# Performance work log

Measured on AMD Instinct MI355X. Metric: run time of the kernel, lower is better.

Reference implementation:

```python
import jax, jax.numpy as jnp
import numpy as np

EMBEDDING_DIM = 64
N_EMBEDDINGS = 512


def setup_inputs() -> dict:
    key = jax.random.key(0)
    k1, k2 = jax.random.split(key)
    inputs = jax.random.normal(k1, (32, 64, 64, 64), dtype=jnp.float32)  # NCHW, C==embedding_dim
    weight = jax.random.normal(k2, (N_EMBEDDINGS, EMBEDDING_DIM), dtype=jnp.float32)
    return {"inputs": inputs, "weight": weight}


def reference(inputs, weight):
    # NCHW -> NHWC, flatten to [N, D]
    x = jnp.transpose(inputs, (0, 2, 3, 1))  # [B, H, W, D]
    in_shape = x.shape
    flat = x.reshape(-1, EMBEDDING_DIM)  # [N, D]

    distances = (
        jnp.sum(flat * flat, axis=1, keepdims=True)
        + jnp.sum(weight * weight, axis=1)
        - 2.0 * flat @ weight.T
    )
    idx = jnp.argmin(distances, axis=1)  # [N]

    # one-hot @ weight is just a gather
    quantized = weight[idx].reshape(in_shape)  # [B, H, W, D]

    # commitment loss: mse(stop_grad(quantized), x)
    e_latent_loss = jnp.mean(jnp.square(jax.lax.stop_gradient(quantized) - x))

    # straight-through estimator
    quantized = x + jax.lax.stop_gradient(quantized - x)

    return jnp.transpose(quantized, (0, 3, 1, 2)), e_latent_loss
```

## Files before the change

### kernel.cpp

```cpp
#include <hip/hip_runtime.h>
#include <math.h>

typedef short bf16x8 __attribute__((ext_vector_type(8)));
typedef float f32x4 __attribute__((ext_vector_type(4)));

#define VQ_D 64
#define VQ_K 512
#define VQ_NQ 131072
#define VQ_TOTAL 8388608
#define NCK 8
#define TAU 8e-3f

typedef __attribute__((address_space(1))) void as1_void;
typedef __attribute__((address_space(3))) void as3_void;

__device__ __forceinline__ void gll16(const void* g, void* l) {
    __builtin_amdgcn_global_load_lds((as1_void*)(void*)g, (as3_void*)l, 16, 0, 0);
}
__device__ __forceinline__ void gll4(const void* g, void* l) {
    __builtin_amdgcn_global_load_lds((as1_void*)(void*)g, (as3_void*)l, 4, 0, 0);
}

__device__ __forceinline__ ushort bf16_rne(float f) {
    uint u = __builtin_bit_cast(uint, f);
    u += 0x7fffu + ((u >> 16) & 1u);
    return (ushort)(u >> 16);
}
__device__ __forceinline__ float bf16_to_f(ushort h) {
    uint u = ((uint)h) << 16;
    return __builtin_bit_cast(float, u);
}
__device__ __forceinline__ uint rne_top(float r) {
    uint t = __builtin_bit_cast(uint, r);
    return t + 0x7fffu + ((t >> 16) & 1u);
}
__device__ __forceinline__ uint pack_hi16(uint a, uint b) {
    return __builtin_amdgcn_perm(b, a, 0x07060302u);
}

__global__ __launch_bounds__(128) void vq_prep(const float* __restrict__ w,
                                               ushort* __restrict__ wfrag,
                                               float* __restrict__ wn,
                                               float* __restrict__ out) {
    if (blockIdx.x == 0 && threadIdx.x == 0) out[VQ_TOTAL] = 0.f;
    const int tid = threadIdx.x;
    const int k = (blockIdx.x << 4) + (tid >> 3);
    const int g = tid & 7;
    const float4* row = (const float4*)(w + k * VQ_D);
    float4 a = row[2 * g], b4 = row[2 * g + 1];
    float v[8] = {a.x, a.y, a.z, a.w, b4.x, b4.y, b4.z, b4.w};
    ushort hi[8], lo[8];
    float nrm = 0.f;
#pragma unroll
    for (int j = 0; j < 8; ++j) {
        nrm = fmaf(v[j], v[j], nrm);
        hi[j] = bf16_rne(v[j]);
        lo[j] = bf16_rne(v[j] - bf16_to_f(hi[j]));
    }
    nrm += __shfl_xor(nrm, 1, 64);
    nrm += __shfl_xor(nrm, 2, 64);
    nrm += __shfl_xor(nrm, 4, 64);
    if (g == 0) wn[k] = nrm;
    const int t = k >> 4, col = k & 15;
    const int quad = g & 3, fh = g >> 2;
    bf16x8* basez = (bf16x8*)wfrag + t * 256 + quad * 16 + col;
    basez[fh * 64]       = *(bf16x8*)hi;
    basez[(2 + fh) * 64] = *(bf16x8*)lo;
}

__global__ __launch_bounds__(512, 4) void vq_main(const float* __restrict__ in,
                                                  const float* __restrict__ w,
                                                  const ushort* __restrict__ wfrag,
                                                  const float* __restrict__ wng,
                                                  float* __restrict__ out) {
    __shared__ __align__(16) char bstage[2][16384];
    __shared__ float wn_lds[VQ_K];
    __shared__ float xn_lds[128];
    __shared__ float pb_lds[2][128], ps_lds[2][128];
    __shared__ int   pi_lds[2][128], pj_lds[2][128];
    __shared__ int   bi_lds[128];
    __shared__ double loss_lds[8];

    const int tid  = threadIdx.x;
    const int lane = tid & 63;
    const int wid  = tid >> 6;
    const int qg   = wid >> 1;
    const int cg   = wid & 1;
    const int col  = lane & 15;
    const int quad = lane >> 4;
    const int n0  = blockIdx.x * 128;
    const int b   = n0 >> 12;
    const int hw0 = n0 & 4095;
    const float* xg0 = in + (b << 18) + hw0;

    {
        const char* gs = (const char*)wfrag + tid * 16;
        char* lb = &bstage[0][0] + wid * 1024;
        gll16(gs, lb);
        gll16(gs + 8192, lb + 8192);
        gll4(wng + tid, (char*)wn_lds + wid * 256);
    }

    bf16x8 ah0[2], ah1[2], al0[2], al1[2];
#pragma unroll
    for (int T = 0; T < 2; ++T) {
        const float* xq = xg0 + qg * 32 + T * 16 + col;
        float sx = 0.f;
        uint AH0[4], AL0[4], AH1[4], AL1[4];
#pragma unroll
        for (int m = 0; m < 4; ++m) {
            float a0 = xq[(quad * 8 + 2 * m) << 12];
            float b0 = xq[(quad * 8 + 2 * m + 1) << 12];
            float a1 = xq[(32 + quad * 8 + 2 * m) << 12];
            float b1 = xq[(32 + quad * 8 + 2 * m + 1) << 12];
            sx = fmaf(a0, a0, sx); sx = fmaf(b0, b0, sx);
            sx = fmaf(a1, a1, sx); sx = fmaf(b1, b1, sx);
            uint ua0 = __builtin_bit_cast(uint, a0), ub0 = __builtin_bit_cast(uint, b0);
            uint ua1 = __builtin_bit_cast(uint, a1), ub1 = __builtin_bit_cast(uint, b1);
            AH0[m] = pack_hi16(ua0, ub0);
            AH1[m] = pack_hi16(ua1, ub1);
            float ha0 = __builtin_bit_cast(float, ua0 & 0xFFFF0000u);
            float hb0 = __builtin_bit_cast(float, ub0 & 0xFFFF0000u);
            float ha1 = __builtin_bit_cast(float, ua1 & 0xFFFF0000u);
            float hb1 = __builtin_bit_cast(float, ub1 & 0xFFFF0000u);
            AL0[m] = pack_hi16(rne_top(a0 - ha0), rne_top(b0 - hb0));
            AL1[m] = pack_hi16(rne_top(a1 - ha1), rne_top(b1 - hb1));
        }
        ah0[T] = *(bf16x8*)AH0; al0[T] = *(bf16x8*)AL0;
        ah1[T] = *(bf16x8*)AH1; al1[T] = *(bf16x8*)AL1;
        sx += __shfl_xor(sx, 16, 64);
        sx += __shfl_xor(sx, 32, 64);
        if (quad == 0) xn_lds[qg * 32 + T * 16 + col] = sx;
    }

    __syncthreads();

    float best[2][4], sec[2][4];
#pragma unroll
    for (int T = 0; T < 2; ++T)
#pragma unroll
        for (int r = 0; r < 4; ++r) { best[T][r] = 3.0e38f; sec[T][r] = 3.0e38f; }

#pragma unroll 1
    for (int c = 0; c < NCK; ++c) {
        char* const bcur = &bstage[c & 1][0];
        if (c + 1 < NCK) {
            const char* gs = (const char*)wfrag + (c + 1) * 16384 + tid * 16;
            char* lb = &bstage[(c + 1) & 1][0] + wid * 1024;
            gll16(gs, lb);
            gll16(gs + 8192, lb + 8192);
        }
#pragma unroll
        for (int s = 0; s < 2; ++s) {
            const int st = cg * 2 + s;
            const int t2 = 4 * c + st;
            const char* rb = bcur + st * 4096 + lane * 16;
            bf16x8 bh0 = *(const bf16x8*)(rb);
            bf16x8 bh1 = *(const bf16x8*)(rb + 1024);
            bf16x8 bl0 = *(const bf16x8*)(rb + 2048);
            bf16x8 bl1 = *(const bf16x8*)(rb + 3072);
            const float wnv = wn_lds[t2 * 16 + col];
#pragma unroll
            for (int T = 0; T < 2; ++T) {
                f32x4 acc = {0.f, 0.f, 0.f, 0.f};
                __builtin_amdgcn_s_setprio(1);
                acc = __builtin_amdgcn_mfma_f32_16x16x32_bf16(ah0[T], bh0, acc, 0, 0, 0);
                acc = __builtin_amdgcn_mfma_f32_16x16x32_bf16(ah1[T], bh1, acc, 0, 0, 0);
                acc = __builtin_amdgcn_mfma_f32_16x16x32_bf16(ah0[T], bl0, acc, 0, 0, 0);
                acc = __builtin_amdgcn_mfma_f32_16x16x32_bf16(ah1[T], bl1, acc, 0, 0, 0);
                acc = __builtin_amdgcn_mfma_f32_16x16x32_bf16(al0[T], bh0, acc, 0, 0, 0);
                acc = __builtin_amdgcn_mfma_f32_16x16x32_bf16(al1[T], bh1, acc, 0, 0, 0);
                __builtin_amdgcn_s_setprio(0);
#pragma unroll
                for (int j = 0; j < 4; ++j) {
                    float dist = fmaf(-2.f, acc[j], wnv);
                    uint u = (__builtin_bit_cast(uint, dist) & 0xFFFFFFE0u)
                           | ((uint)t2 & 0x1Fu);
                    float key = __builtin_bit_cast(float, u);
                    float m = fmaxf(best[T][j], key);
                    best[T][j] = fminf(best[T][j], key);
                    sec[T][j]  = fminf(sec[T][j], m);
                }
            }
        }
        __syncthreads();
    }

    float bD[2][4], sD[2][4];
    int bI[2][4], sI[2][4];
#pragma unroll
    for (int T = 0; T < 2; ++T)
#pragma unroll
    for (int r = 0; r < 4; ++r) {
        uint ub = __builtin_bit_cast(uint, best[T][r]);
        uint us = __builtin_bit_cast(uint, sec[T][r]);
        bI[T][r] = (int)(ub & 31u) * 16 + col;
        sI[T][r] = (int)(us & 31u) * 16 + col;
        bD[T][r] = __builtin_bit_cast(float, ub & 0xFFFFFFE0u);
        sD[T][r] = __builtin_bit_cast(float, us & 0xFFFFFFE0u);
    }

#pragma unroll
    for (int off = 1; off < 16; off <<= 1) {
#pragma unroll
        for (int T = 0; T < 2; ++T)
#pragma unroll
        for (int r = 0; r < 4; ++r) {
            float ob = __shfl_xor(bD[T][r], off, 64);
            float os = __shfl_xor(sD[T][r], off, 64);
            int   oi = __shfl_xor(bI[T][r], off, 64);
            int   oc = __shfl_xor(sI[T][r], off, 64);
            bool oWins = (ob < bD[T][r]) || (ob == bD[T][r] && oi < bI[T][r]);
            float nb  = oWins ? ob       : bD[T][r];
            int   ni  = oWins ? oi       : bI[T][r];
            float c1  = oWins ? bD[T][r] : ob;
            int   ci1 = oWins ? bI[T][r] : oi;
            float c2  = oWins ? os       : sD[T][r];
            int   ci2 = oWins ? oc       : sI[T][r];
            bool c1w = (c1 < c2) || (c1 == c2 && ci1 < ci2);
            sD[T][r] = c1w ? c1  : c2;
            sI[T][r] = c1w ? ci1 : ci2;
            bD[T][r] = nb; bI[T][r] = ni;
        }
    }
    if (col == 0) {
#pragma unroll
        for (int T = 0; T < 2; ++T)
#pragma unroll
        for (int r = 0; r < 4; ++r) {
            const int q = qg * 32 + T * 16 + quad * 4 + r;
            pb_lds[cg][q] = bD[T][r]; ps_lds[cg][q] = sD[T][r];
            pi_lds[cg][q] = bI[T][r]; pj_lds[cg][q] = sI[T][r];
        }
    }
    __syncthreads();

    {
        const int q = tid >> 2, part = tid & 3;
        float b0 = pb_lds[0][q], b1 = pb_lds[1][q];
        float s0 = ps_lds[0][q], s1 = ps_lds[1][q];
        int   i0 = pi_lds[0][q], i1 = pi_lds[1][q];
        int   j0 = pj_lds[0][q], j1 = pj_lds[1][q];
        bool w0 = (b0 < b1) || (b0 == b1 && i0 < i1);
        float cb  = w0 ? b0 : b1;  int cbi = w0 ? i0 : i1;
        float c1  = w0 ? b1 : b0;  int ci1 = w0 ? i1 : i0;
        float c2  = w0 ? s0 : s1;  int ci2 = w0 ? j0 : j1;
        bool c1w = (c1 < c2) || (c1 == c2 && ci1 < ci2);
        float cs  = c1w ? c1 : c2; int csi = c1w ? ci1 : ci2;

        double chosen = (double)cb;
        if (cs - cb < TAU) {
            const float* wb  = w + cbi * VQ_D + part * 16;
            const float* ws2 = w + csi * VQ_D + part * 16;
            const float* xqp = xg0 + q;
            double nb = 0.0, dotb = 0.0, ns = 0.0, dots = 0.0;
#pragma unroll
            for (int d0 = 0; d0 < 16; ++d0) {
                const int d = part * 16 + d0;
                double xv = (double)xqp[d << 12];
                double wbv = (double)wb[d0], wsv = (double)ws2[d0];
                nb = fma(wbv, wbv, nb); dotb = fma(xv, wbv, dotb);
                ns = fma(wsv, wsv, ns); dots = fma(xv, wsv, dots);
            }
#pragma unroll
            for (int off = 1; off < 4; off <<= 1) {
                nb   += __shfl_xor(nb,   off, 64);
                dotb += __shfl_xor(dotb, off, 64);
                ns   += __shfl_xor(ns,   off, 64);
                dots += __shfl_xor(dots, off, 64);
            }
            double db = nb - 2.0 * dotb, ds = ns - 2.0 * dots;
            if (ds < db || (ds == db && csi < cbi)) { cbi = csi; chosen = ds; }
            else                                    { chosen = db; }
        }
        if (part == 0) bi_lds[q] = cbi;
        double lq = (part == 0) ? ((double)xn_lds[q] + chosen) : 0.0;
#pragma unroll
        for (int off = 32; off > 0; off >>= 1)
            lq += __shfl_down(lq, off, 64);
        if (lane == 0) loss_lds[wid] = lq;
    }
    __syncthreads();
    if (tid == 0) {
        double s = 0.0;
#pragma unroll
        for (int wv = 0; wv < 8; ++wv) s += loss_lds[wv];
        atomicAdd(out + VQ_TOTAL, (float)(s * (1.0 / (double)VQ_TOTAL)));
    }

    {
        const int q = tid & 127, quarter = tid >> 7;
        const float4* wrow = (const float4*)(w + bi_lds[q] * VQ_D) + quarter * 4;
        float* op = out + (b << 18) + hw0 + q;
#pragma unroll
        for (int u = 0; u < 4; ++u) {
            float4 v = wrow[u];
            const int d = quarter * 16 + 4 * u;
            op[(d + 0) << 12] = v.x;
            op[(d + 1) << 12] = v.y;
            op[(d + 2) << 12] = v.z;
            op[(d + 3) << 12] = v.w;
        }
    }
}

extern "C" void kernel_launch(void* const* d_in, const int* in_sizes, int n_in,
                              void* d_out, int out_size, void* d_ws, size_t ws_size,
                              hipStream_t stream) {
    const float* in = (const float*)d_in[0];
    const float* w  = (const float*)d_in[1];
    float* out = (float*)d_out;

    ushort* wfrag = (ushort*)d_ws;
    float*  wn    = (float*)((char*)d_ws + 131072);

    vq_prep<<<32, 128, 0, stream>>>(w, wfrag, wn, out);
    vq_main<<<VQ_NQ / 128, 512, 0, stream>>>(in, w, wfrag, wn, out);
}
```

Before: 126.4 us.

## Give each wave the full codebook and double queries per block

Each block now processes 256 queries instead of 128, and every wave scans all 512 codebook entries for its own 32 queries instead of splitting the codebook between two waves. This halves the codebook staging and LDS fragment reads per query and removes the cross-wave best/second-best merge through LDS. The second-best update is also folded into a single fmed3 instruction. In exchange the grid shrinks to half as many blocks, which lowers the number of resident waves available to hide latency, and each wave runs a longer serial MFMA loop.

```diff
diff --git a/kernel.cpp b/kernel.cpp
--- a/kernel.cpp
+++ b/kernel.cpp
@@ -9,6 +9,7 @@
 #define VQ_NQ 131072
 #define VQ_TOTAL 8388608
 #define NCK 8
+#define QB 256
 #define TAU 8e-3f
 
 typedef __attribute__((address_space(1))) void as1_void;
@@ -75,20 +76,17 @@
                                                   float* __restrict__ out) {
     __shared__ __align__(16) char bstage[2][16384];
     __shared__ float wn_lds[VQ_K];
-    __shared__ float xn_lds[128];
-    __shared__ float pb_lds[2][128], ps_lds[2][128];
-    __shared__ int   pi_lds[2][128], pj_lds[2][128];
-    __shared__ int   bi_lds[128];
+    __shared__ float xn_lds[QB];
+    __shared__ float best_lds[QB], sec_lds[QB];
+    __shared__ int   bi_lds[QB], si_lds[QB];
     __shared__ double loss_lds[8];
 
     const int tid  = threadIdx.x;
     const int lane = tid & 63;
     const int wid  = tid >> 6;
-    const int qg   = wid >> 1;
-    const int cg   = wid & 1;
     const int col  = lane & 15;
     const int quad = lane >> 4;
-    const int n0  = blockIdx.x * 128;
+    const int n0  = blockIdx.x * QB;
     const int b   = n0 >> 12;
     const int hw0 = n0 & 4095;
     const float* xg0 = in + (b << 18) + hw0;
@@ -104,7 +102,7 @@
     bf16x8 ah0[2], ah1[2], al0[2], al1[2];
 #pragma unroll
     for (int T = 0; T < 2; ++T) {
-        const float* xq = xg0 + qg * 32 + T * 16 + col;
+        const float* xq = xg0 + wid * 32 + T * 16 + col;
         float sx = 0.f;
         uint AH0[4], AL0[4], AH1[4], AL1[4];
 #pragma unroll
@@ -130,7 +128,7 @@
         ah1[T] = *(bf16x8*)AH1; al1[T] = *(bf16x8*)AL1;
         sx += __shfl_xor(sx, 16, 64);
         sx += __shfl_xor(sx, 32, 64);
-        if (quad == 0) xn_lds[qg * 32 + T * 16 + col] = sx;
+        if (quad == 0) xn_lds[wid * 32 + T * 16 + col] = sx;
     }
 
     __syncthreads();
@@ -151,10 +149,9 @@
             gll16(gs + 8192, lb + 8192);
         }
 #pragma unroll
-        for (int s = 0; s < 2; ++s) {
-            const int st = cg * 2 + s;
-            const int t2 = 4 * c + st;
-            const char* rb = bcur + st * 4096 + lane * 16;
+        for (int s = 0; s < 4; ++s) {
+            const int t2 = 4 * c + s;
+            const char* rb = bcur + s * 4096 + lane * 16;
             bf16x8 bh0 = *(const bf16x8*)(rb);
             bf16x8 bh1 = *(const bf16x8*)(rb + 1024);
             bf16x8 bl0 = *(const bf16x8*)(rb + 2048);
@@ -177,9 +174,8 @@
                     uint u = (__builtin_bit_cast(uint, dist) & 0xFFFFFFE0u)
                            | ((uint)t2 & 0x1Fu);
                     float key = __builtin_bit_cast(float, u);
-                    float m = fmaxf(best[T][j], key);
+                    sec[T][j]  = __builtin_amdgcn_fmed3f(best[T][j], sec[T][j], key);
                     best[T][j] = fminf(best[T][j], key);
-                    sec[T][j]  = fminf(sec[T][j], m);
                 }
             }
         }
@@ -228,47 +224,35 @@
         for (int T = 0; T < 2; ++T)
 #pragma unroll
         for (int r = 0; r < 4; ++r) {
-            const int q = qg * 32 + T * 16 + quad * 4 + r;
-            pb_lds[cg][q] = bD[T][r]; ps_lds[cg][q] = sD[T][r];
-            pi_lds[cg][q] = bI[T][r]; pj_lds[cg][q] = sI[T][r];
+            const int q = wid * 32 + T * 16 + quad * 4 + r;
+            best_lds[q] = bD[T][r]; sec_lds[q] = sD[T][r];
+            bi_lds[q] = bI[T][r];   si_lds[q] = sI[T][r];
         }
     }
     __syncthreads();
 
     {
-        const int q = tid >> 2, part = tid & 3;
-        float b0 = pb_lds[0][q], b1 = pb_lds[1][q];
-        float s0 = ps_lds[0][q], s1 = ps_lds[1][q];
-        int   i0 = pi_lds[0][q], i1 = pi_lds[1][q];
-        int   j0 = pj_lds[0][q], j1 = pj_lds[1][q];
-        bool w0 = (b0 < b1) || (b0 == b1 && i0 < i1);
-        float cb  = w0 ? b0 : b1;  int cbi = w0 ? i0 : i1;
-        float c1  = w0 ? b1 : b0;  int ci1 = w0 ? i1 : i0;
-        float c2  = w0 ? s0 : s1;  int ci2 = w0 ? j0 : j1;
-        bool c1w = (c1 < c2) || (c1 == c2 && ci1 < ci2);
-        float cs  = c1w ? c1 : c2; int csi = c1w ? ci1 : ci2;
-
+        const int q = tid >> 1, part = tid & 1;
+        float cb = best_lds[q], cs = sec_lds[q];
+        int cbi = bi_lds[q], csi = si_lds[q];
         double chosen = (double)cb;
         if (cs - cb < TAU) {
-            const float* wb  = w + cbi * VQ_D + part * 16;
-            const float* ws2 = w + csi * VQ_D + part * 16;
+            const float* wb  = w + cbi * VQ_D + part * 32;
+            const float* ws2 = w + csi * VQ_D + part * 32;
             const float* xqp = xg0 + q;
             double nb = 0.0, dotb = 0.0, ns = 0.0, dots = 0.0;
 #pragma unroll
-            for (int d0 = 0; d0 < 16; ++d0) {
-                const int d = part * 16 + d0;
+            for (int d0 = 0; d0 < 32; ++d0) {
+                const int d = part * 32 + d0;
                 double xv = (double)xqp[d << 12];
                 double wbv = (double)wb[d0], wsv = (double)ws2[d0];
                 nb = fma(wbv, wbv, nb); dotb = fma(xv, wbv, dotb);
                 ns = fma(wsv, wsv, ns); dots = fma(xv, wsv, dots);
             }
-#pragma unroll
-            for (int off = 1; off < 4; off <<= 1) {
-                nb   += __shfl_xor(nb,   off, 64);
-                dotb += __shfl_xor(dotb, off, 64);
-                ns   += __shfl_xor(ns,   off, 64);
-                dots += __shfl_xor(dots, off, 64);
-            }
+            nb   += __shfl_xor(nb,   1, 64);
+            dotb += __shfl_xor(dotb, 1, 64);
+            ns   += __shfl_xor(ns,   1, 64);
+            dots += __shfl_xor(dots, 1, 64);
             double db = nb - 2.0 * dotb, ds = ns - 2.0 * dots;
             if (ds < db || (ds == db && csi < cbi)) { cbi = csi; chosen = ds; }
             else                                    { chosen = db; }
@@ -289,13 +273,13 @@
     }
 
     {
-        const int q = tid & 127, quarter = tid >> 7;
-        const float4* wrow = (const float4*)(w + bi_lds[q] * VQ_D) + quarter * 4;
+        const int q = tid & 255, half = tid >> 8;
+        const float4* wrow = (const float4*)(w + bi_lds[q] * VQ_D) + half * 8;
         float* op = out + (b << 18) + hw0 + q;
 #pragma unroll
-        for (int u = 0; u < 4; ++u) {
+        for (int u = 0; u < 8; ++u) {
             float4 v = wrow[u];
-            const int d = quarter * 16 + 4 * u;
+            const int d = half * 32 + 4 * u;
             op[(d + 0) << 12] = v.x;
             op[(d + 1) << 12] = v.y;
             op[(d + 2) << 12] = v.z;
@@ -315,5 +299,5 @@
     float*  wn    = (float*)((char*)d_ws + 131072);
 
     vq_prep<<<32, 128, 0, stream>>>(w, wfrag, wn, out);
-    vq_main<<<VQ_NQ / 128, 512, 0, stream>>>(in, w, wfrag, wn, out);
-}
+    vq_main<<<VQ_NQ / QB, 512, 0, stream>>>(in, w, wfrag, wn, out);
+}
```

Result: faster. 118.8 us (-6.0%).
